# Optimization experiments

Measured on AMD Instinct MI355X. Metric: run time of the kernel, lower is better.

## Reference

```python
import jax, jax.numpy as jnp
import numpy as np

H = 2048        # hidden_size
NH = 16         # num query heads
NKV = 4         # num kv heads
HD = 128        # head_dim
EPS = 1e-6
SCALE = HD ** -0.5
GROUPS = NH // NKV


def rotate_half(x):
    x1, x2 = x[..., : HD // 2], x[..., HD // 2:]
    return jnp.concatenate((-x2, x1), axis=-1)


def rmsnorm(x, w):
    # x: [..., HD]
    var = jnp.mean(jnp.square(x), axis=-1, keepdims=True)
    return x * jax.lax.rsqrt(var + EPS) * w


def setup_inputs() -> dict:
    key = jax.random.key(0)
    ks = jax.random.split(key, 10)
    B, QL, CL = 4, 1024, 3072
    s = 0.02
    return {
        "noise": jax.random.normal(ks[0], (B, QL, H), jnp.float32),
        "ctx": jax.random.normal(ks[1], (B, CL, H), jnp.float32),
        "cos": jax.random.uniform(ks[2], (B, CL + QL, HD), jnp.float32, -1.0, 1.0),
        "sin": jax.random.uniform(ks[3], (B, CL + QL, HD), jnp.float32, -1.0, 1.0),
        "Wq": jax.random.normal(ks[4], (H, NH * HD), jnp.float32) * s,
        "Wk": jax.random.normal(ks[5], (H, NKV * HD), jnp.float32) * s,
        "Wv": jax.random.normal(ks[6], (H, NKV * HD), jnp.float32) * s,
        "Wo": jax.random.normal(ks[7], (NH * HD, H), jnp.float32) * s,
        "qn_w": jnp.ones((HD,), jnp.float32),
        "kn_w": jnp.ones((HD,), jnp.float32),
    }


def reference(noise, ctx, cos, sin, Wq, Wk, Wv, Wo, qn_w, kn_w):
    B, QL, _ = noise.shape
    CL = ctx.shape[1]
    KL = CL + QL

    # Q from noise
    q = (noise @ Wq).reshape(B, QL, NH, HD)
    q = rmsnorm(q, qn_w).transpose(0, 2, 1, 3)            # [B, NH, QL, HD]

    # K/V from [ctx ; noise]
    kv_in = jnp.concatenate([ctx, noise], axis=1)          # [B, KL, H]
    k = (kv_in @ Wk).reshape(B, KL, NKV, HD)
    k = rmsnorm(k, kn_w).transpose(0, 2, 1, 3)             # [B, NKV, KL, HD]
    v = (kv_in @ Wv).reshape(B, KL, NKV, HD).transpose(0, 2, 1, 3)

    # RoPE: queries use last QL positions
    cos_q, sin_q = cos[:, -QL:, None].transpose(0, 2, 1, 3), sin[:, -QL:, None].transpose(0, 2, 1, 3)
    cos_k, sin_k = cos[:, None], sin[:, None]
    q = q * cos_q + rotate_half(q) * sin_q
    k = k * cos_k + rotate_half(k) * sin_k

    # GQA expansion
    k = jnp.repeat(k, GROUPS, axis=1)                      # [B, NH, KL, HD]
    v = jnp.repeat(v, GROUPS, axis=1)

    attn = jnp.einsum('bhqd,bhkd->bhqk', q, k) * SCALE     # [B, NH, QL, KL]
    attn = jax.nn.softmax(attn.astype(jnp.float32), axis=-1).astype(v.dtype)
    out = jnp.einsum('bhqk,bhkd->bhqd', attn, v)
    out = out.transpose(0, 2, 1, 3).reshape(B, QL, NH * HD)
    return out @ Wo
```

## Files before the change

### kernel.cpp

```cpp
#include <hip/hip_runtime.h>
#include <cstdint>
#include <cstddef>

#define DEVI __device__ __forceinline__

typedef short bf16x8 __attribute__((ext_vector_type(8)));
typedef short bf16x4 __attribute__((ext_vector_type(4)));
typedef float f32x4  __attribute__((ext_vector_type(4)));

constexpr int H_  = 2048;
constexpr int NH  = 16;
constexpr int NKV = 4;
constexpr int HD  = 128;
constexpr int B_  = 4;
constexpr int QL  = 1024;
constexpr int CL  = 3072;
constexpr int KL  = 4096;
constexpr float EPS = 1e-6f;
constexpr float SCALE_LOG2E = 0.08838834764831845f * 1.4426950408889634f;

DEVI unsigned short f2bf(float x) {
  unsigned int u = __float_as_uint(x);
  u += 0x7FFFu + ((u >> 16) & 1u);
  return (unsigned short)(u >> 16);
}
DEVI float bf2f(unsigned short u) {
  return __uint_as_float(((unsigned int)u) << 16);
}
DEVI bf16x4 mk4(float a, float b, float c, float d) {
  unsigned ua = __float_as_uint(a) + 0x8000u, ub = __float_as_uint(b) + 0x8000u;
  unsigned uc = __float_as_uint(c) + 0x8000u, ud = __float_as_uint(d) + 0x8000u;
  union { unsigned u[2]; bf16x4 v; } r;
  r.u[0] = __builtin_amdgcn_perm(ub, ua, 0x07060302u);
  r.u[1] = __builtin_amdgcn_perm(ud, uc, 0x07060302u);
  return r.v;
}

DEVI void async16(const void* g, void* l) {
  __builtin_amdgcn_global_load_lds(
      (const __attribute__((address_space(1))) void*)g,
      (__attribute__((address_space(3))) void*)l, 16, 0, 0);
}

__global__ __launch_bounds__(256)
void prep(const float* __restrict__ noise, const float* __restrict__ ctx,
          unsigned short* __restrict__ kvin) {
  const size_t t = (size_t)blockIdx.x * 256 + threadIdx.x;
  const size_t e = t * 8;
  const int row = (int)(e / H_), col = (int)(e % H_);
  const int b = row >> 12, pos = row & 4095;
  const float* src = (pos < CL) ? ctx + ((size_t)(b * CL + pos)) * H_ + col
                                : noise + ((size_t)(b * QL + (pos - CL))) * H_ + col;
  float4 x = ((const float4*)src)[0], y = ((const float4*)src)[1];
  bf16x8 v;
  v[0] = (short)f2bf(x.x); v[1] = (short)f2bf(x.y);
  v[2] = (short)f2bf(x.z); v[3] = (short)f2bf(x.w);
  v[4] = (short)f2bf(y.x); v[5] = (short)f2bf(y.y);
  v[6] = (short)f2bf(y.z); v[7] = (short)f2bf(y.w);
  *(bf16x8*)(kvin + e) = v;
}

__global__ __launch_bounds__(256)
void wtrans(const float* __restrict__ in, unsigned short* __restrict__ out,
            int K, int N) {
  __shared__ float t[64][65];
  const int ktiles = K >> 6;
  const int kt = blockIdx.x % ktiles;
  const int nt = blockIdx.x / ktiles;
  {
    const int r = threadIdx.x >> 2, cs = threadIdx.x & 3;
    const float4* src = (const float4*)(in + (size_t)(kt * 64 + r) * N + nt * 64 + cs * 16);
    #pragma unroll
    for (int i = 0; i < 4; ++i) {
      float4 v = src[i];
      t[r][cs * 16 + i * 4 + 0] = v.x;
      t[r][cs * 16 + i * 4 + 1] = v.y;
      t[r][cs * 16 + i * 4 + 2] = v.z;
      t[r][cs * 16 + i * 4 + 3] = v.w;
    }
  }
  __syncthreads();
  {
    const int n = threadIdx.x >> 2, ks = threadIdx.x & 3;
    bf16x8 o0, o1;
    #pragma unroll
    for (int i = 0; i < 8; ++i) o0[i] = (short)f2bf(t[ks * 16 + i][n]);
    #pragma unroll
    for (int i = 0; i < 8; ++i) o1[i] = (short)f2bf(t[ks * 16 + 8 + i][n]);
    unsigned short* op = out + (size_t)(nt * 64 + n) * K + kt * 64 + ks * 16;
    *(bf16x8*)(op) = o0;
    *(bf16x8*)(op + 8) = o1;
  }
}

template <int MODE>
__global__ __launch_bounds__(256)
void gemm2(const unsigned short* __restrict__ Abf,
           const unsigned short* __restrict__ Bt,
           const float* __restrict__ normw,
           const float* __restrict__ cosb, const float* __restrict__ sinb,
           unsigned short* __restrict__ outb, float* __restrict__ outf) {
  constexpr int M  = (MODE == 1 || MODE == 2) ? (B_ * KL) : (B_ * QL);
  constexpr int K  = H_;
  constexpr int MT = M / 128;

  __shared__ union U {
    struct { unsigned short a[128][64]; unsigned short b[128][64]; } st;
    unsigned short ct[128][138];
  } sm;

  const int tid  = threadIdx.x;
  const int tm   = blockIdx.x % MT;
  const int tn   = blockIdx.x / MT;
  const int wid  = tid >> 6, lane = tid & 63, quad = lane >> 4, lm = lane & 15;
  const int wm   = wid >> 1, wn = wid & 1;

  f32x4 acc[4][4];
  #pragma unroll
  for (int i = 0; i < 4; ++i)
    #pragma unroll
    for (int j = 0; j < 4; ++j)
      #pragma unroll
      for (int r = 0; r < 4; ++r) acc[i][j][r] = 0.f;

  const unsigned short* agp[4];
  const unsigned short* bgp[4];
  #pragma unroll
  for (int i = 0; i < 4; ++i) {
    const int idx = i * 256 + tid;
    const int arow = idx >> 3, g = idx & 7, gg = g ^ (arow & 7);
    int grow;
    if constexpr (MODE == 0) {
      const int gmr = tm * 128 + arow;
      grow = (gmr >> 10) * KL + CL + (gmr & 1023);
    } else {
      grow = tm * 128 + arow;
    }
    agp[i] = Abf + (size_t)grow * K + gg * 8;
    bgp[i] = Bt + (size_t)(tn * 128 + arow) * K + gg * 8;
  }

  for (int kt = 0; kt < K / 64; ++kt) {
    __syncthreads();
    #pragma unroll
    for (int i = 0; i < 4; ++i) {
      async16(agp[i] + kt * 64, (char*)&sm.st.a[0][0] + (i * 256 + wid * 64) * 16);
      async16(bgp[i] + kt * 64, (char*)&sm.st.b[0][0] + (i * 256 + wid * 64) * 16);
    }
    __syncthreads();
    #pragma unroll
    for (int ks = 0; ks < 2; ++ks) {
      bf16x8 af[4], bfr[4];
      #pragma unroll
      for (int i = 0; i < 4; ++i) {
        const int swz = (ks * 4 + quad) ^ (lm & 7);
        af[i] = *(const bf16x8*)&sm.st.a[wm * 64 + i * 16 + lm][swz * 8];
      }
      #pragma unroll
      for (int j = 0; j < 4; ++j) {
        const int swz = (ks * 4 + quad) ^ (lm & 7);
        bfr[j] = *(const bf16x8*)&sm.st.b[wn * 64 + j * 16 + lm][swz * 8];
      }
      #pragma unroll
      for (int i = 0; i < 4; ++i)
        #pragma unroll
        for (int j = 0; j < 4; ++j)
          acc[i][j] = __builtin_amdgcn_mfma_f32_16x16x32_bf16(af[i], bfr[j], acc[i][j], 0, 0, 0);
    }
  }

  if constexpr (MODE == 3) {
    #pragma unroll
    for (int i = 0; i < 4; ++i)
      #pragma unroll
      for (int j = 0; j < 4; ++j) {
        const int row = tm * 128 + wm * 64 + i * 16 + quad * 4;
        const int col = tn * 128 + wn * 64 + j * 16 + lm;
        #pragma unroll
        for (int rr = 0; rr < 4; ++rr)
          outf[(size_t)(row + rr) * H_ + col] = acc[i][j][rr];
      }
    return;
  }

  __syncthreads();
  #pragma unroll
  for (int i = 0; i < 4; ++i)
    #pragma unroll
    for (int j = 0; j < 4; ++j)
      #pragma unroll
      for (int rr = 0; rr < 4; ++rr)
        sm.ct[wm * 64 + i * 16 + quad * 4 + rr][wn * 64 + j * 16 + lm] =
            f2bf(acc[i][j][rr]);
  __syncthreads();

  const int row2 = tid >> 1, half = tid & 1;
  if constexpr (MODE == 0 || MODE == 1) {
    const int gmr = tm * 128 + row2;
    int ci; size_t obase;
    if constexpr (MODE == 0) {
      const int b = gmr >> 10, pos = gmr & 1023;
      ci = (b * KL + CL + pos) * HD;
      obase = ((size_t)((b * NH + tn) * QL + pos)) * HD;
    } else {
      const int b = gmr >> 12, pos = gmr & 4095;
      ci = (b * KL + pos) * HD;
      obase = ((size_t)((b * NKV + tn) * KL + pos)) * HD;
    }
    float ss = 0.f;
    for (int d = half * 64; d < half * 64 + 64; ++d) {
      float v = bf2f(sm.ct[row2][d]);
      ss += v * v;
    }
    ss += __shfl_xor(ss, 1);
    const float rinv = rsqrtf(ss * (1.0f / 128.0f) + EPS);
    constexpr float OSC = (MODE == 0) ? SCALE_LOG2E : 1.0f;
    #pragma unroll
    for (int d8 = 0; d8 < 8; ++d8) {
      bf16x8 v;
      #pragma unroll
      for (int j = 0; j < 8; ++j) {
        const int d = half * 64 + d8 * 8 + j;
        const float x  = bf2f(sm.ct[row2][d])      * rinv * normw[d];
        const float xo = bf2f(sm.ct[row2][d ^ 64]) * rinv * normw[d ^ 64];
        const float rot = (d < 64) ? -xo : xo;
        v[j] = (short)f2bf((x * cosb[ci + d] + rot * sinb[ci + d]) * OSC);
      }
      *(bf16x8*)(outb + obase + half * 64 + d8 * 8) = v;
    }
  } else {
    const int d = row2;
    const int b = (tm * 128) >> 12;
    const int posBase = ((tm * 128) & 4095) + half * 64;
    const size_t obase = ((size_t)((b * NKV + tn) * HD + d)) * KL + posBase;
    #pragma unroll
    for (int k8 = 0; k8 < 8; ++k8) {
      bf16x8 v;
      #pragma unroll
      for (int j = 0; j < 8; ++j)
        v[j] = (short)sm.ct[half * 64 + k8 * 8 + j][d];
      *(bf16x8*)(outb + obase + k8 * 8) = v;
    }
  }
}

__global__ __launch_bounds__(256, 4)
void attn2(const unsigned short* __restrict__ qb,
           const unsigned short* __restrict__ kb,
           const unsigned short* __restrict__ vtb,
           unsigned short* __restrict__ ao) {
  __shared__ unsigned short kl[64][128];
  __shared__ unsigned short vl[128][64];

  const int tid = threadIdx.x;
  const int wave = tid >> 6, lane = tid & 63, quad = lane >> 4, lm = lane & 15;
  const int qblk = blockIdx.x & 15;
  const int bh = blockIdx.x >> 4;
  const int b = bh >> 4, h = bh & 15, kvh = h >> 2;
  const int q0 = qblk * 64 + wave * 16;

  bf16x8 qf[4];
  const unsigned short* qbase = qb + ((size_t)((b * NH + h) * QL + q0)) * HD;
  #pragma unroll
  for (int kq = 0; kq < 4; ++kq)
    qf[kq] = *(const bf16x8*)(qbase + lm * HD + kq * 32 + quad * 8);

  f32x4 o[8];
  float li = 0.f;
  #pragma unroll
  for (int dt = 0; dt < 8; ++dt)
    #pragma unroll
    for (int rr = 0; rr < 4; ++rr) o[dt][rr] = 0.f;

  const unsigned short* kbase = kb + ((size_t)(b * NKV + kvh)) * KL * HD;
  const unsigned short* vbase = vtb + ((size_t)(b * NKV + kvh)) * HD * KL;

  const unsigned short* kgp[4];
  const unsigned short* vgp[4];
  #pragma unroll
  for (int i = 0; i < 4; ++i) {
    const int idx = i * 256 + tid;
    const int krow = idx >> 4, gc = idx & 15;
    const int gg = (gc & 8) | ((gc & 7) ^ (krow & 7));
    kgp[i] = kbase + (size_t)krow * HD + gg * 8;
    const int vrow = idx >> 3, g = idx & 7;
    const int gv = g ^ (vrow & 7);
    vgp[i] = vbase + (size_t)vrow * KL + gv * 8;
  }

  for (int kt = 0; kt < KL / 64; ++kt) {
    __syncthreads();
    #pragma unroll
    for (int i = 0; i < 4; ++i) {
      async16(kgp[i] + (size_t)kt * 64 * HD, (char*)&kl[0][0] + (i * 256 + wave * 64) * 16);
      async16(vgp[i] + kt * 64,              (char*)&vl[0][0] + (i * 256 + wave * 64) * 16);
    }
    __syncthreads();

    #pragma unroll
    for (int nt = 0; nt < 4; ++nt) {
      bf16x8 kf[4];
      #pragma unroll
      for (int kq = 0; kq < 4; ++kq) {
        const int gc = kq * 4 + quad;
        const int swz = (gc & 8) | ((gc & 7) ^ (lm & 7));
        kf[kq] = *(const bf16x8*)&kl[nt * 16 + lm][swz * 8];
      }
      f32x4 s0 = {0.f, 0.f, 0.f, 0.f};
      __builtin_amdgcn_s_setprio(1);
      #pragma unroll
      for (int kq = 0; kq < 4; ++kq)
        s0 = __builtin_amdgcn_mfma_f32_16x16x32_bf16(kf[kq], qf[kq], s0, 0, 0, 0);
      __builtin_amdgcn_s_setprio(0);
      float e00 = __builtin_amdgcn_exp2f(s0[0]), e01 = __builtin_amdgcn_exp2f(s0[1]);
      float e02 = __builtin_amdgcn_exp2f(s0[2]), e03 = __builtin_amdgcn_exp2f(s0[3]);
      li += (e00 + e01) + (e02 + e03);
      bf16x4 p0 = mk4(e00, e01, e02, e03);
      __builtin_amdgcn_s_setprio(1);
      #pragma unroll
      for (int dt = 0; dt < 8; ++dt) {
        const int gv = (nt * 2 + (quad >> 1)) ^ (lm & 7);
        bf16x4 vf = *(const bf16x4*)&vl[dt * 16 + lm][gv * 8 + (quad & 1) * 4];
        o[dt] = __builtin_amdgcn_mfma_f32_16x16x16bf16_1k(vf, p0, o[dt], 0, 0, 0);
      }
      __builtin_amdgcn_s_setprio(0);
    }
  }

  {
    float l = li;
    l += __shfl_xor(l, 16);
    l += __shfl_xor(l, 32);
    const float inv = 1.0f / l;
    const size_t rowbase = ((size_t)(b * QL + q0 + lm)) * (NH * HD) + h * HD;
    #pragma unroll
    for (int dt = 0; dt < 8; ++dt) {
      bf16x4 v = mk4(o[dt][0] * inv, o[dt][1] * inv,
                     o[dt][2] * inv, o[dt][3] * inv);
      *(bf16x4*)(ao + rowbase + dt * 16 + quad * 4) = v;
    }
  }
}

extern "C" void kernel_launch(void* const* d_in, const int* in_sizes, int n_in,
                              void* d_out, int out_size, void* d_ws, size_t ws_size,
                              hipStream_t stream) {
  const float* noise = (const float*)d_in[0];
  const float* ctx   = (const float*)d_in[1];
  const float* cosb  = (const float*)d_in[2];
  const float* sinb  = (const float*)d_in[3];
  const float* Wq    = (const float*)d_in[4];
  const float* Wk    = (const float*)d_in[5];
  const float* Wv    = (const float*)d_in[6];
  const float* Wo    = (const float*)d_in[7];
  const float* qn    = (const float*)d_in[8];
  const float* kn    = (const float*)d_in[9];
  float* out = (float*)d_out;

  char* ws = (char*)d_ws;
  unsigned short* kvin = (unsigned short*)(ws);
  unsigned short* aob  = (unsigned short*)(ws);
  unsigned short* WqT  = (unsigned short*)(ws + 67108864);
  unsigned short* WkT  = (unsigned short*)(ws + 67108864 + 8388608);
  unsigned short* WvT  = (unsigned short*)(ws + 67108864 + 10485760);
  unsigned short* WoT  = (unsigned short*)(ws + 67108864 + 12582912);
  unsigned short* qbuf = (unsigned short*)(ws + 67108864 + 20971520);
  unsigned short* kbuf = (unsigned short*)(ws + 67108864 + 37748736);
  unsigned short* vtb  = (unsigned short*)(ws + 67108864 + 54525952);

  prep<<<dim3((B_ * KL * H_) / 8 / 256), dim3(256), 0, stream>>>(noise, ctx, kvin);

  wtrans<<<dim3(1024), dim3(256), 0, stream>>>(Wq, WqT, 2048, 2048);
  wtrans<<<dim3(256),  dim3(256), 0, stream>>>(Wk, WkT, 2048, 512);
  wtrans<<<dim3(256),  dim3(256), 0, stream>>>(Wv, WvT, 2048, 512);
  wtrans<<<dim3(1024), dim3(256), 0, stream>>>(Wo, WoT, 2048, 2048);

  gemm2<0><<<dim3(32 * 16), dim3(256), 0, stream>>>(
      kvin, WqT, qn, cosb, sinb, qbuf, nullptr);
  gemm2<1><<<dim3(128 * 4), dim3(256), 0, stream>>>(
      kvin, WkT, kn, cosb, sinb, kbuf, nullptr);
  gemm2<2><<<dim3(128 * 4), dim3(256), 0, stream>>>(
      kvin, WvT, nullptr, nullptr, nullptr, vtb, nullptr);

  attn2<<<dim3(1024), dim3(256), 0, stream>>>(qbuf, kbuf, vtb, aob);

  gemm2<3><<<dim3(32 * 16), dim3(256), 0, stream>>>(
      aob, WoT, nullptr, nullptr, nullptr, nullptr, out);
}
```

Baseline: 638.2 us.

## Enlarge attention query tile per wave and double-buffer K/V staging

Each wave now handles 64 query rows instead of 16, so every K/V tile loaded into LDS is reused across four query subtiles, and the grid shrinks from 1024 to 256 blocks. K/V loads are double-buffered, with the next tile's async copies issued before computing on the current one and synchronised through vmcnt waits and raw barriers. This targets global and LDS load traffic and load latency. In exchange, register pressure rises sharply (four sets of accumulators plus Q fragments, with launch bounds lowered to one block), and 256 blocks may underfill the GPU's compute units.

```diff
diff --git a/kernel.cpp b/kernel.cpp
--- a/kernel.cpp
+++ b/kernel.cpp
@@ -244,58 +244,68 @@
   }
 }
 
-__global__ __launch_bounds__(256, 4)
+__global__ __launch_bounds__(256, 1)
 void attn2(const unsigned short* __restrict__ qb,
            const unsigned short* __restrict__ kb,
            const unsigned short* __restrict__ vtb,
            unsigned short* __restrict__ ao) {
-  __shared__ unsigned short kl[64][128];
-  __shared__ unsigned short vl[128][64];
+  __shared__ unsigned short kl[2][64][128];
+  __shared__ unsigned short vl[2][128][64];
 
   const int tid = threadIdx.x;
   const int wave = tid >> 6, lane = tid & 63, quad = lane >> 4, lm = lane & 15;
-  const int qblk = blockIdx.x & 15;
-  const int bh = blockIdx.x >> 4;
+  const int qblk = blockIdx.x & 3;
+  const int bh = blockIdx.x >> 2;
   const int b = bh >> 4, h = bh & 15, kvh = h >> 2;
-  const int q0 = qblk * 64 + wave * 16;
-
-  bf16x8 qf[4];
+  const int q0 = qblk * 256 + wave * 64;
+
+  bf16x8 qf[4][4];
   const unsigned short* qbase = qb + ((size_t)((b * NH + h) * QL + q0)) * HD;
   #pragma unroll
-  for (int kq = 0; kq < 4; ++kq)
-    qf[kq] = *(const bf16x8*)(qbase + lm * HD + kq * 32 + quad * 8);
-
-  f32x4 o[8];
-  float li = 0.f;
-  #pragma unroll
-  for (int dt = 0; dt < 8; ++dt)
-    #pragma unroll
-    for (int rr = 0; rr < 4; ++rr) o[dt][rr] = 0.f;
+  for (int t = 0; t < 4; ++t)
+    #pragma unroll
+    for (int kq = 0; kq < 4; ++kq)
+      qf[t][kq] = *(const bf16x8*)(qbase + (t * 16 + lm) * HD + kq * 32 + quad * 8);
+
+  f32x4 o[4][8];
+  float li[4] = {0.f, 0.f, 0.f, 0.f};
+  #pragma unroll
+  for (int t = 0; t < 4; ++t)
+    #pragma unroll
+    for (int dt = 0; dt < 8; ++dt)
+      #pragma unroll
+      for (int rr = 0; rr < 4; ++rr) o[t][dt][rr] = 0.f;
 
   const unsigned short* kbase = kb + ((size_t)(b * NKV + kvh)) * KL * HD;
   const unsigned short* vbase = vtb + ((size_t)(b * NKV + kvh)) * HD * KL;
 
-  const unsigned short* kgp[4];
-  const unsigned short* vgp[4];
-  #pragma unroll
-  for (int i = 0; i < 4; ++i) {
-    const int idx = i * 256 + tid;
-    const int krow = idx >> 4, gc = idx & 15;
-    const int gg = (gc & 8) | ((gc & 7) ^ (krow & 7));
-    kgp[i] = kbase + (size_t)krow * HD + gg * 8;
-    const int vrow = idx >> 3, g = idx & 7;
-    const int gv = g ^ (vrow & 7);
-    vgp[i] = vbase + (size_t)vrow * KL + gv * 8;
-  }
-
+  const int krow0 = tid >> 4, kgc = tid & 15;
+  const int kgg = (kgc & 8) | ((kgc & 7) ^ (krow0 & 7));
+  const unsigned short* kgp0 = kbase + (size_t)krow0 * HD + kgg * 8;
+  const int vrow0 = tid >> 3;
+  const int vgv = (tid & 7) ^ (vrow0 & 7);
+  const unsigned short* vgp0 = vbase + (size_t)vrow0 * KL + vgv * 8;
+
+  auto stage = [&](int bufi, int ktt) {
+    #pragma unroll
+    for (int i = 0; i < 4; ++i) {
+      async16(kgp0 + (size_t)ktt * (64 * HD) + i * (16 * HD),
+              (char*)&kl[bufi][0][0] + (i * 256 + wave * 64) * 16);
+      async16(vgp0 + (size_t)ktt * 64 + i * (32 * KL),
+              (char*)&vl[bufi][0][0] + (i * 256 + wave * 64) * 16);
+    }
+  };
+
+  stage(0, 0);
   for (int kt = 0; kt < KL / 64; ++kt) {
-    __syncthreads();
-    #pragma unroll
-    for (int i = 0; i < 4; ++i) {
-      async16(kgp[i] + (size_t)kt * 64 * HD, (char*)&kl[0][0] + (i * 256 + wave * 64) * 16);
-      async16(vgp[i] + kt * 64,              (char*)&vl[0][0] + (i * 256 + wave * 64) * 16);
-    }
-    __syncthreads();
+    const int cur = kt & 1;
+    if (kt + 1 < KL / 64) {
+      stage(cur ^ 1, kt + 1);
+      asm volatile("s_waitcnt vmcnt(8)" ::: "memory");
+    } else {
+      asm volatile("s_waitcnt vmcnt(0)" ::: "memory");
+    }
+    __builtin_amdgcn_s_barrier();
 
     #pragma unroll
     for (int nt = 0; nt < 4; ++nt) {
@@ -304,39 +314,51 @@
       for (int kq = 0; kq < 4; ++kq) {
         const int gc = kq * 4 + quad;
         const int swz = (gc & 8) | ((gc & 7) ^ (lm & 7));
-        kf[kq] = *(const bf16x8*)&kl[nt * 16 + lm][swz * 8];
-      }
-      f32x4 s0 = {0.f, 0.f, 0.f, 0.f};
-      __builtin_amdgcn_s_setprio(1);
-      #pragma unroll
-      for (int kq = 0; kq < 4; ++kq)
-        s0 = __builtin_amdgcn_mfma_f32_16x16x32_bf16(kf[kq], qf[kq], s0, 0, 0, 0);
-      __builtin_amdgcn_s_setprio(0);
-      float e00 = __builtin_amdgcn_exp2f(s0[0]), e01 = __builtin_amdgcn_exp2f(s0[1]);
-      float e02 = __builtin_amdgcn_exp2f(s0[2]), e03 = __builtin_amdgcn_exp2f(s0[3]);
-      li += (e00 + e01) + (e02 + e03);
-      bf16x4 p0 = mk4(e00, e01, e02, e03);
-      __builtin_amdgcn_s_setprio(1);
+        kf[kq] = *(const bf16x8*)&kl[cur][nt * 16 + lm][swz * 8];
+      }
+      bf16x4 vf[8];
       #pragma unroll
       for (int dt = 0; dt < 8; ++dt) {
         const int gv = (nt * 2 + (quad >> 1)) ^ (lm & 7);
-        bf16x4 vf = *(const bf16x4*)&vl[dt * 16 + lm][gv * 8 + (quad & 1) * 4];
-        o[dt] = __builtin_amdgcn_mfma_f32_16x16x16bf16_1k(vf, p0, o[dt], 0, 0, 0);
-      }
-      __builtin_amdgcn_s_setprio(0);
-    }
-  }
-
-  {
-    float l = li;
+        vf[dt] = *(const bf16x4*)&vl[cur][dt * 16 + lm][gv * 8 + (quad & 1) * 4];
+      }
+      f32x4 s[4];
+      #pragma unroll
+      for (int t = 0; t < 4; ++t)
+        #pragma unroll
+        for (int rr = 0; rr < 4; ++rr) s[t][rr] = 0.f;
+      #pragma unroll
+      for (int kq = 0; kq < 4; ++kq)
+        #pragma unroll
+        for (int t = 0; t < 4; ++t)
+          s[t] = __builtin_amdgcn_mfma_f32_16x16x32_bf16(kf[kq], qf[t][kq], s[t], 0, 0, 0);
+      #pragma unroll
+      for (int t = 0; t < 4; ++t) {
+        float e0 = __builtin_amdgcn_exp2f(s[t][0]);
+        float e1 = __builtin_amdgcn_exp2f(s[t][1]);
+        float e2 = __builtin_amdgcn_exp2f(s[t][2]);
+        float e3 = __builtin_amdgcn_exp2f(s[t][3]);
+        li[t] += (e0 + e1) + (e2 + e3);
+        bf16x4 p = mk4(e0, e1, e2, e3);
+        #pragma unroll
+        for (int dt = 0; dt < 8; ++dt)
+          o[t][dt] = __builtin_amdgcn_mfma_f32_16x16x16bf16_1k(vf[dt], p, o[t][dt], 0, 0, 0);
+      }
+    }
+    __builtin_amdgcn_s_barrier();
+  }
+
+  #pragma unroll
+  for (int t = 0; t < 4; ++t) {
+    float l = li[t];
     l += __shfl_xor(l, 16);
     l += __shfl_xor(l, 32);
     const float inv = 1.0f / l;
-    const size_t rowbase = ((size_t)(b * QL + q0 + lm)) * (NH * HD) + h * HD;
+    const size_t rowbase = ((size_t)(b * QL + q0 + t * 16 + lm)) * (NH * HD) + h * HD;
     #pragma unroll
     for (int dt = 0; dt < 8; ++dt) {
-      bf16x4 v = mk4(o[dt][0] * inv, o[dt][1] * inv,
-                     o[dt][2] * inv, o[dt][3] * inv);
+      bf16x4 v = mk4(o[t][dt][0] * inv, o[t][dt][1] * inv,
+                     o[t][dt][2] * inv, o[t][dt][3] * inv);
       *(bf16x4*)(ao + rowbase + dt * 16 + quad * 4) = v;
     }
   }
@@ -382,7 +404,7 @@
   gemm2<2><<<dim3(128 * 4), dim3(256), 0, stream>>>(
       kvin, WvT, nullptr, nullptr, nullptr, vtb, nullptr);
 
-  attn2<<<dim3(1024), dim3(256), 0, stream>>>(qbuf, kbuf, vtb, aob);
+  attn2<<<dim3(256), dim3(256), 0, stream>>>(qbuf, kbuf, vtb, aob);
 
   gemm2<3><<<dim3(32 * 16), dim3(256), 0, stream>>>(
       aob, WoT, nullptr, nullptr, nullptr, nullptr, out);
```

Measured after the change: 636.3 us. Within noise of the previous version (-0.3%).
